# Performance work log

Measured on AMD Instinct MI355X. Metric: run time of the kernel, lower is better.

## Reference

```python
import jax, jax.numpy as jnp
import numpy as np

B, H, W = 2, 256, 256
C_BB = 1029          # concatenated deeplab backbone channels
FEATURE_DIM = 20     # output_conv emits FEATURE_DIM-5; +3 color +2 coords
NSPIX_H = NSPIX_W = 16
NSPIX = NSPIX_H * NSPIX_W
N_ITER = 10
HW = H * W


def _conv_bn_relu(x, Wc, g, b, eps=1e-5):
    # Conv2d(3x3, pad=1, bias=False) + BatchNorm2d (training stats) + ReLU
    y = jax.lax.conv_general_dilated(x, Wc, (1, 1), 'SAME',
                                     dimension_numbers=('NCHW', 'OIHW', 'NCHW'))
    mu = y.mean((0, 2, 3), keepdims=True)
    var = ((y - mu) ** 2).mean((0, 2, 3), keepdims=True)
    y = (y - mu) * jax.lax.rsqrt(var + eps)
    y = y * g.reshape(1, -1, 1, 1) + b.reshape(1, -1, 1, 1)
    return jnp.maximum(y, 0.0)


def _candidates():
    # init label map (nearest-neighbor upsample of the 16x16 superpixel grid)
    r0 = (jnp.arange(H) * NSPIX_H) // H
    c0 = (jnp.arange(W) * NSPIX_W) // W
    d = jnp.array([-1, 0, 1])
    dr, dc = jnp.meshgrid(d, d, indexing='ij')   # 3x3 superpixel neighborhood
    dr = dr.reshape(9); dc = dc.reshape(9)
    cr = r0[None, :, None] + dr[:, None, None]   # [9,H,1]
    cc = c0[None, None, :] + dc[:, None, None]   # [9,1,W]
    valid = (cr >= 0) & (cr < NSPIX_H) & (cc >= 0) & (cc < NSPIX_W)
    cid = jnp.clip(cr, 0, NSPIX_H - 1) * NSPIX_W + jnp.clip(cc, 0, NSPIX_W - 1)
    cid = jnp.broadcast_to(cid, (9, H, W)).reshape(9, HW)
    valid = jnp.broadcast_to(valid, (9, H, W)).reshape(9, HW)
    return cid, valid


def _ssn_iter(pixel_f):
    Bq, C = pixel_f.shape[0], pixel_f.shape[1]
    cid, valid = _candidates()
    ids = cid.reshape(-1)                         # [9*HW]
    validf = valid[None].astype(pixel_f.dtype)    # [1,9,HW]
    pf = pixel_f.reshape(Bq, C, HW)
    pfT = pf.transpose(0, 2, 1)                   # [B,HW,C]
    # init centroids = adaptive_avg_pool2d to the superpixel grid
    cent = pixel_f.reshape(Bq, C, NSPIX_H, H // NSPIX_H, NSPIX_W, W // NSPIX_W).mean((3, 5)).reshape(Bq, C, NSPIX)
    neg_inf = jnp.asarray(-jnp.inf, pixel_f.dtype)

    def update(wb, pb):  # wb [9,HW], pb [HW,C] -> new centroids [C,K]
        dat = (wb[:, :, None] * pb[None, :, :]).reshape(9 * HW, C)
        num = jax.ops.segment_sum(dat, ids, num_segments=NSPIX)
        den = jax.ops.segment_sum(wb.reshape(-1), ids, num_segments=NSPIX)
        return (num / (den[:, None] + 1e-16)).T

    aff = None
    for _ in range(N_ITER):
        cc = cent[:, :, cid]                                      # [B,C,9,HW]
        dist = jnp.sum((pf[:, :, None, :] - cc) ** 2, axis=1)     # [B,9,HW]
        aff = jax.nn.softmax(jnp.where(valid[None], -dist, neg_inf), axis=1)
        w = aff * validf
        cent = jax.vmap(update)(w, pfT)
    return aff, cid, cent


def setup_inputs() -> dict:
    key = jax.random.key(0)
    ks = jax.random.split(key, 6)
    x = jax.random.normal(ks[0], (B, 3, H, W), jnp.float32)
    yy, xx = jnp.meshgrid(jnp.arange(H, dtype=jnp.float32),
                          jnp.arange(W, dtype=jnp.float32), indexing='ij')
    coords = jnp.broadcast_to(jnp.stack([yy, xx])[None], (B, 2, H, W))
    feats = jax.random.normal(ks[1], (B, C_BB, H, W), jnp.float32)

    def cw(k, o, i):
        return jax.random.normal(k, (o, i, 3, 3), jnp.float32) * (1.0 / np.sqrt(9.0 * i))

    return dict(x=x, coords=coords, feats=feats,
                W1=cw(ks[2], 500, C_BB), g1=jnp.ones(500), b1=jnp.zeros(500),
                W2=cw(ks[3], 100, 500), g2=jnp.ones(100), b2=jnp.zeros(100),
                W3=cw(ks[4], FEATURE_DIM - 5, 100), g3=jnp.ones(FEATURE_DIM - 5), b3=jnp.zeros(FEATURE_DIM - 5))


def reference(x, coords, feats, W1, g1, b1, W2, g2, b2, W3, g3, b3):
    h = _conv_bn_relu(feats, W1, g1, b1)
    h = _conv_bn_relu(h, W2, g2, b2)
    h = _conv_bn_relu(h, W3, g3, b3)
    pixel_f = jnp.concatenate([h, x, coords], axis=1)  # [B,FEATURE_DIM,H,W]
    return _ssn_iter(pixel_f)
```

## Files before the change

### kernel.cpp

```cpp
#include <hip/hip_runtime.h>
#include <math.h>

#define kB 2
#define kH 256
#define kW 256
#define kHW 65536
#define kHp 258
#define kWp 258
#define kNSPIX 256
#define kC 20
#define kNITER 10

typedef unsigned int uint;
typedef unsigned short ushort;

using f32x4  = __attribute__((ext_vector_type(4))) float;
using bf16x8 = __attribute__((ext_vector_type(8))) __bf16;

__device__ __forceinline__ ushort f2bf(float f) {
    uint u = __float_as_uint(f);
    u = (u + 0x7FFFu + ((u >> 16) & 1u)) >> 16;
    return (ushort)u;
}
__device__ __forceinline__ float bf2f(uint h) {
    return __uint_as_float(h << 16);
}

__device__ __forceinline__ void gld16(const void* g, void* l) {
    __builtin_amdgcn_global_load_lds(
        (const __attribute__((address_space(1))) unsigned int*)g,
        (__attribute__((address_space(3))) unsigned int*)l, 16, 0, 0);
}

__global__ __launch_bounds__(256) void xtrans(
    const float* __restrict__ src, ushort* __restrict__ dst,
    int Cin_real, int Cin_pad)
{
    __shared__ float s[64][33];
    const int ci0 = blockIdx.x * 32;
    const int p0  = blockIdx.y * 64;
    const int b   = blockIdx.z;
    const int tid = threadIdx.x;
    for (int e = tid; e < 2048; e += 256) {
        int ci = e >> 6, px = e & 63;
        int cig = ci0 + ci;
        float v = 0.f;
        if (cig < Cin_real) v = src[((long)b * Cin_real + cig) * kHW + p0 + px];
        s[px][ci] = v;
    }
    __syncthreads();
    const int px = tid >> 2, g = tid & 3;
    uint4 o;
    o.x = (uint)f2bf(s[px][g*8+0]) | ((uint)f2bf(s[px][g*8+1]) << 16);
    o.y = (uint)f2bf(s[px][g*8+2]) | ((uint)f2bf(s[px][g*8+3]) << 16);
    o.z = (uint)f2bf(s[px][g*8+4]) | ((uint)f2bf(s[px][g*8+5]) << 16);
    o.w = (uint)f2bf(s[px][g*8+6]) | ((uint)f2bf(s[px][g*8+7]) << 16);
    const int y = p0 >> 8;
    const int x = (p0 & 255) + px;
    *(uint4*)(dst + ((long)(b * kHp + y + 1) * kWp + x + 1) * Cin_pad + ci0 + g * 8) = o;
}

__global__ __launch_bounds__(256) void wtrans(
    const float* __restrict__ W, ushort* __restrict__ Wt,
    int Cout_real, int Cin_real, int Cout_pad, int Cin_pad)
{
    long idx = (long)blockIdx.x * 256 + threadIdx.x;
    long total = (long)9 * Cout_pad * Cin_pad;
    if (idx >= total) return;
    int t   = (int)(idx / ((long)Cout_pad * Cin_pad));
    long r  = idx - (long)t * Cout_pad * Cin_pad;
    int co  = (int)(r / Cin_pad);
    int ci  = (int)(r - (long)co * Cin_pad);
    float v = 0.f;
    if (co < Cout_real && ci < Cin_real) v = W[((long)co * Cin_real + ci) * 9 + t];
    Wt[idx] = f2bf(v);
}

__global__ __launch_bounds__(256) void zero_border(ushort* __restrict__ buf, int Cpad)
{
    int e = blockIdx.x * 256 + threadIdx.x;
    if (e >= 1028) return;
    int gq = blockIdx.y;
    int b  = blockIdx.z;
    int y, x;
    if (e < 516) { y = (e < 258) ? 0 : 257; x = (e < 258) ? e : e - 258; }
    else         { int f = e - 516; y = 1 + (f >> 1); x = (f & 1) ? 257 : 0; }
    uint4 z = {0u, 0u, 0u, 0u};
    *(uint4*)(buf + ((long)(b * kHp + y) * kWp + x) * Cpad + (long)gq * 8) = z;
}

__global__ __launch_bounds__(256, 3) void conv_mfma(
    const ushort* __restrict__ Xt, const ushort* __restrict__ Wt,
    ushort* __restrict__ Yt, float* __restrict__ stats,
    int Cin_pad, int Cout_pad, int nkc)
{
    __shared__ __align__(16) ushort As[2][6144];
    __shared__ __align__(16) ushort Bs[2][4608];

    const int tid  = threadIdx.x;
    const int lane = tid & 63;
    const int wave = tid >> 6;
    const int l15  = lane & 15;
    const int quad = lane >> 4;
    const int co_w = (wave >> 1) * 32;
    const int px_w = (wave & 1) * 64;
    const int co0  = blockIdx.x * 64;
    const int py   = blockIdx.y >> 1;
    const int x0   = (blockIdx.y & 1) * 128;
    const int b    = blockIdx.z;
    const int ca8  = (quad ^ ((l15 >> 1) & 3)) * 8;

    f32x4 acc[2][4];
    #pragma unroll
    for (int i = 0; i < 2; ++i)
        #pragma unroll
        for (int j = 0; j < 4; ++j) acc[i][j] = (f32x4)0.0f;

    auto stage = [&](int s, int kyv, int ci0) {
        const ushort* xrow = Xt + ((long)(b * kHp + py + kyv) * kWp + x0) * Cin_pad + ci0;
        ushort* bd = &Bs[s][0];
        {
            int u = tid;        int px = u >> 2, gs = u & 3;
            gld16(xrow + (long)px * Cin_pad + ((gs ^ ((px >> 1) & 3)) * 8), bd + u * 8);
        }
        {
            int u = tid + 256;  int px = u >> 2, gs = u & 3;
            gld16(xrow + (long)px * Cin_pad + ((gs ^ ((px >> 1) & 3)) * 8), bd + u * 8);
        }
        if (tid < 64) {
            int u = tid + 512;  int px = u >> 2; px = px > 129 ? 129 : px;
            int gs = u & 3;
            gld16(xrow + (long)px * Cin_pad + ((gs ^ ((px >> 1) & 3)) * 8), bd + u * 8);
        }
        const ushort* wb = Wt + ((long)(kyv * 3) * Cout_pad + co0) * Cin_pad + ci0;
        ushort* ad = &As[s][0];
        #pragma unroll
        for (int r = 0; r < 3; ++r) {
            int u = tid + r * 256;
            int tl = u >> 8, co = (u >> 2) & 63, gs = u & 3;
            gld16(wb + ((long)tl * Cout_pad + co) * Cin_pad + ((gs ^ ((co >> 1) & 3)) * 8), ad + u * 8);
        }
    };

    int ky = 0, cc = 0;
    stage(0, 0, 0);
    const int NCH = 3 * nkc;
    for (int q = 0; q < NCH; ++q) {
        const int s = q & 1;
        int ky_n = ky, cc_n = cc + 1;
        if (cc_n == nkc) { cc_n = 0; ++ky_n; }
        if (q + 1 < NCH) {
            stage(s ^ 1, ky_n, cc_n * 32);
            asm volatile("s_waitcnt vmcnt(5)" ::: "memory");
        } else {
            asm volatile("s_waitcnt vmcnt(0)" ::: "memory");
        }
        __builtin_amdgcn_s_barrier();
        asm volatile("" ::: "memory");

        const ushort* Ab = &As[s][0];
        const ushort* Bb = &Bs[s][0];
        #pragma unroll
        for (int kx = 0; kx < 3; ++kx) {
            bf16x8 a0 = *(const bf16x8*)(Ab + (kx * 64 + co_w + l15) * 32 + ca8);
            bf16x8 a1 = *(const bf16x8*)(Ab + (kx * 64 + co_w + 16 + l15) * 32 + ca8);
            #pragma unroll
            for (int j = 0; j < 4; ++j) {
                int px = px_w + j * 16 + l15 + kx;
                bf16x8 bb = *(const bf16x8*)(Bb + px * 32 + ((quad ^ ((px >> 1) & 3)) * 8));
                acc[0][j] = __builtin_amdgcn_mfma_f32_16x16x32_bf16(a0, bb, acc[0][j], 0, 0, 0);
                acc[1][j] = __builtin_amdgcn_mfma_f32_16x16x32_bf16(a1, bb, acc[1][j], 0, 0, 0);
            }
        }
        asm volatile("s_waitcnt lgkmcnt(0)" ::: "memory");
        __builtin_amdgcn_s_barrier();
        asm volatile("" ::: "memory");
        ky = ky_n; cc = cc_n;
    }

    const long rowbase = (long)(b * kHp + py + 1) * kWp + x0 + 1 + px_w;
    #pragma unroll
    for (int i = 0; i < 2; ++i) {
        #pragma unroll
        for (int reg = 0; reg < 4; ++reg) {
            int co_r = co0 + co_w + i * 16 + quad * 4 + reg;
            float s = 0.f, s2 = 0.f;
            #pragma unroll
            for (int j = 0; j < 4; ++j) {
                float v = acc[i][j][reg];
                s += v;
                s2 = fmaf(v, v, s2);
                Yt[(rowbase + j * 16 + l15) * Cout_pad + co_r] = f2bf(v);
            }
            #pragma unroll
            for (int off = 1; off <= 8; off <<= 1) {
                s  += __shfl_xor(s, off);
                s2 += __shfl_xor(s2, off);
            }
            if (l15 == 0) {
                atomicAdd(&stats[co_r], s);
                atomicAdd(&stats[Cout_pad + co_r], s2);
            }
        }
    }
}

__global__ void finalize_stats(const float* __restrict__ stats,
                               float* __restrict__ murs, int Cout_pad)
{
    int c = blockIdx.x * 256 + threadIdx.x;
    if (c >= Cout_pad) return;
    const float invN = 1.0f / (float)(kB * kHW);
    float mu  = stats[c] * invN;
    float var = stats[Cout_pad + c] * invN - mu * mu;
    murs[c] = mu;
    murs[Cout_pad + c] = rsqrtf(var + 1e-5f);
}

__global__ __launch_bounds__(256) void bn_relu_nhwc(
    ushort* __restrict__ Y, const float* __restrict__ murs,
    const float* __restrict__ g, const float* __restrict__ bia,
    int C_real, int C_pad)
{
    long idx = (long)blockIdx.x * 256 + threadIdx.x;
    const int ngc = C_pad >> 3;
    long total = (long)kB * kHW * ngc;
    if (idx >= total) return;
    int cg = (int)(idx % ngc);
    long p  = idx / ngc;
    int b  = (int)(p >> 16);
    int pp = (int)(p & 65535);
    int y = pp >> 8, x = pp & 255;
    ushort* ptr = Y + ((long)(b * kHp + y + 1) * kWp + x + 1) * C_pad + (long)cg * 8;
    uint4 v = *(uint4*)ptr;
    uint w[4] = {v.x, v.y, v.z, v.w};
    uint o[4];
    #pragma unroll
    for (int q = 0; q < 4; ++q) {
        int c0 = cg * 8 + q * 2;
        int c1 = c0 + 1;
        float f0 = 0.f, f1 = 0.f;
        if (c0 < C_real)
            f0 = fmaxf((bf2f(w[q] & 0xFFFFu) - murs[c0]) * murs[C_pad + c0] * g[c0] + bia[c0], 0.f);
        if (c1 < C_real)
            f1 = fmaxf((bf2f(w[q] >> 16) - murs[c1]) * murs[C_pad + c1] * g[c1] + bia[c1], 0.f);
        o[q] = (uint)f2bf(f0) | ((uint)f2bf(f1) << 16);
    }
    uint4 ov = {o[0], o[1], o[2], o[3]};
    *(uint4*)ptr = ov;
}

__global__ __launch_bounds__(256) void bn_to_pf(
    const ushort* __restrict__ y3, const float* __restrict__ murs,
    const float* __restrict__ g, const float* __restrict__ bia,
    float* __restrict__ pf)
{
    long idx = (long)blockIdx.x * 256 + threadIdx.x;
    if (idx >= (long)kB * 15 * kHW) return;
    int b  = (int)(idx / (15 * kHW));
    long r = idx - (long)b * 15 * kHW;
    int ch = (int)(r / kHW);
    long p = r - (long)ch * kHW;
    int y = (int)(p >> 8), x = (int)(p & 255);
    float v = bf2f((uint)y3[((long)(b * kHp + y + 1) * kWp + x + 1) * 64 + ch]);
    v = fmaxf((v - murs[ch]) * murs[64 + ch] * g[ch] + bia[ch], 0.f);
    pf[((long)b * kC + ch) * kHW + p] = v;
}

__global__ __launch_bounds__(256) void fill_extra(
    const float* __restrict__ x, const float* __restrict__ coords, float* __restrict__ pf)
{
    long idx = (long)blockIdx.x * 256 + threadIdx.x;
    if (idx >= (long)kB * 5 * kHW) return;
    int b   = (int)(idx / (5 * kHW));
    long rem = idx - (long)b * 5 * kHW;
    int c   = (int)(rem / kHW);
    long p  = rem - (long)c * kHW;
    float v = (c < 3) ? x[((long)b * 3 + c) * kHW + p]
                      : coords[((long)b * 2 + (c - 3)) * kHW + p];
    pf[((long)b * kC + 15 + c) * kHW + p] = v;
}

__global__ __launch_bounds__(256) void cid_kernel(float* __restrict__ out_cid)
{
    int idx = blockIdx.x * 256 + threadIdx.x;
    if (idx >= 9 * kHW) return;
    int k = idx / kHW, p = idx - k * kHW;
    int r = p >> 8, c = p & 255;
    int rr = (r >> 4) + k / 3 - 1;
    int cc = (c >> 4) + k % 3 - 1;
    rr = rr < 0 ? 0 : (rr > 15 ? 15 : rr);
    cc = cc < 0 ? 0 : (cc > 15 ? 15 : cc);
    out_cid[idx] = (float)(rr * 16 + cc);
}

__global__ __launch_bounds__(256) void cent_init(
    const float* __restrict__ pf, float* __restrict__ cent)
{
    int idx = blockIdx.x * 256 + threadIdx.x;
    if (idx >= kB * kC * kNSPIX) return;
    int b   = idx / (kC * kNSPIX);
    int rem = idx - b * (kC * kNSPIX);
    int c   = rem / kNSPIX;
    int s   = rem - c * kNSPIX;
    int sr = s >> 4, sc = s & 15;
    const float* base = pf + ((long)b * kC + c) * kHW;
    float sum = 0.f;
    for (int ry = 0; ry < 16; ++ry)
        for (int rx = 0; rx < 16; ++rx)
            sum += base[(sr * 16 + ry) * kW + sc * 16 + rx];
    cent[idx] = sum * (1.0f / 256.0f);
}

__global__ __launch_bounds__(256) void ssn_softmax(
    const float* __restrict__ pf, const float* __restrict__ cent, float* __restrict__ aff)
{
    __shared__ float s_cent[kC][kNSPIX];
    const int b   = blockIdx.y;
    const int tid = threadIdx.x;
    const float* cb = cent + (long)b * kC * kNSPIX;
    for (int i = tid; i < kC * kNSPIX; i += 256)
        s_cent[i >> 8][i & 255] = cb[i];
    __syncthreads();

    const int p  = blockIdx.x * 256 + tid;
    const int r  = p >> 8, c = p & 255;
    const int r0 = r >> 4, c0 = c >> 4;

    float f[kC];
    const float* pb = pf + (long)b * kC * kHW + p;
    #pragma unroll
    for (int ch = 0; ch < kC; ++ch) f[ch] = pb[(long)ch * kHW];

    float dist[9];
    bool  val[9];
    float mx = -1e30f;
    #pragma unroll
    for (int k = 0; k < 9; ++k) {
        int rr = r0 + k / 3 - 1;
        int cc = c0 + k % 3 - 1;
        bool v = (rr >= 0 && rr < 16 && cc >= 0 && cc < 16);
        val[k] = v;
        int sid = v ? rr * 16 + cc : 0;
        float d = 0.f;
        #pragma unroll
        for (int ch = 0; ch < kC; ++ch) {
            float t = f[ch] - s_cent[ch][sid];
            d = fmaf(t, t, d);
        }
        dist[k] = d;
        if (v) mx = fmaxf(mx, -d);
    }
    float e[9], sum = 0.f;
    #pragma unroll
    for (int k = 0; k < 9; ++k) {
        e[k] = val[k] ? expf(-dist[k] - mx) : 0.f;
        sum += e[k];
    }
    float inv = 1.0f / sum;
    float* ab = aff + (long)b * 9 * kHW + p;
    #pragma unroll
    for (int k = 0; k < 9; ++k) ab[(long)k * kHW] = e[k] * inv;
}

__global__ __launch_bounds__(256) void ssn_update(
    const float* __restrict__ pf, const float* __restrict__ aff, float* __restrict__ cent)
{
    const int b  = blockIdx.y;
    const int s  = blockIdx.x;
    const int sr = s >> 4, sc = s & 15;
    const int tid = threadIdx.x;
    const int ty = tid >> 4, tx = tid & 15;

    float acc[kC + 1];
    #pragma unroll
    for (int i = 0; i <= kC; ++i) acc[i] = 0.f;

    #pragma unroll
    for (int k = 0; k < 9; ++k) {
        int dr = k / 3 - 1, dc = k % 3 - 1;
        int br = sr - dr, bc = sc - dc;
        if (br < 0 || br > 15 || bc < 0 || bc > 15) continue;
        int p = (br * 16 + ty) * kW + bc * 16 + tx;
        float w = aff[((long)b * 9 + k) * kHW + p];
        const float* pb = pf + (long)b * kC * kHW + p;
        acc[kC] += w;
        #pragma unroll
        for (int ch = 0; ch < kC; ++ch)
            acc[ch] = fmaf(w, pb[(long)ch * kHW], acc[ch]);
    }

    #pragma unroll
    for (int off = 32; off >= 1; off >>= 1)
        #pragma unroll
        for (int ch = 0; ch <= kC; ++ch)
            acc[ch] += __shfl_down(acc[ch], off);

    __shared__ float part[4][kC + 1];
    int wid = tid >> 6;
    if ((tid & 63) == 0)
        #pragma unroll
        for (int ch = 0; ch <= kC; ++ch) part[wid][ch] = acc[ch];
    __syncthreads();
    if (tid < kC) {
        float num = part[0][tid] + part[1][tid] + part[2][tid] + part[3][tid];
        float den = part[0][kC] + part[1][kC] + part[2][kC] + part[3][kC];
        cent[((long)b * kC + tid) * kNSPIX + s] = num / (den + 1e-16f);
    }
}

extern "C" void kernel_launch(void* const* d_in, const int* in_sizes, int n_in,
                              void* d_out, int out_size, void* d_ws, size_t ws_size,
                              hipStream_t stream)
{
    const float* x      = (const float*)d_in[0];
    const float* coords = (const float*)d_in[1];
    const float* feats  = (const float*)d_in[2];
    const float* W1 = (const float*)d_in[3];
    const float* g1 = (const float*)d_in[4];
    const float* b1 = (const float*)d_in[5];
    const float* W2 = (const float*)d_in[6];
    const float* g2 = (const float*)d_in[7];
    const float* b2 = (const float*)d_in[8];
    const float* W3 = (const float*)d_in[9];
    const float* g3 = (const float*)d_in[10];
    const float* b3 = (const float*)d_in[11];

    const long HPWP = (long)kHp * kWp;
    char* ws = (char*)d_ws;
    ushort* Xt1 = (ushort*)ws;  ws += (long)kB * HPWP * 1056 * 2;
    ushort* Wt1 = (ushort*)ws;  ws += (long)9 * 512 * 1056 * 2;
    ushort* y1t = (ushort*)ws;  ws += (long)kB * HPWP * 512 * 2;
    ushort* Wt2 = (ushort*)ws;  ws += (long)9 * 128 * 512 * 2;
    ushort* y2t = (ushort*)ws;  ws += (long)kB * HPWP * 128 * 2;
    ushort* Wt3 = (ushort*)ws;  ws += (long)9 * 64 * 128 * 2;
    ushort* y3t = (ushort*)ws;  ws += (long)kB * HPWP * 64 * 2;
    float*  pf  = (float*)ws;   ws += (long)2 * kC * kHW * 4;
    float* stats1 = (float*)ws; ws += 1024 * 4;
    float* stats2 = (float*)ws; ws += 256 * 4;
    float* stats3 = (float*)ws; ws += 128 * 4;
    float* murs1  = (float*)ws; ws += 1024 * 4;
    float* murs2  = (float*)ws; ws += 256 * 4;
    float* murs3  = (float*)ws; ws += 128 * 4;

    hipMemsetAsync(stats1, 0, (1024 + 256 + 128 + 1024 + 256 + 128) * 4, stream);

    float* aff_out  = (float*)d_out;
    float* cid_out  = aff_out + (long)kB * 9 * kHW;
    float* cent_out = cid_out + (long)9 * kHW;

    zero_border<<<dim3(5, 132, kB), 256, 0, stream>>>(Xt1, 1056);
    zero_border<<<dim3(5,  64, kB), 256, 0, stream>>>(y1t, 512);
    zero_border<<<dim3(5,  16, kB), 256, 0, stream>>>(y2t, 128);

    xtrans<<<dim3(33, 1024, kB), 256, 0, stream>>>(feats, Xt1, 1029, 1056);
    wtrans<<<(int)(((long)9 * 512 * 1056 + 255) / 256), 256, 0, stream>>>(W1, Wt1, 500, 1029, 512, 1056);
    wtrans<<<(int)(((long)9 * 128 * 512 + 255) / 256), 256, 0, stream>>>(W2, Wt2, 100, 500, 128, 512);
    wtrans<<<(int)(((long)9 * 64 * 128 + 255) / 256), 256, 0, stream>>>(W3, Wt3, 15, 100, 64, 128);

    conv_mfma<<<dim3(8, 512, kB), 256, 0, stream>>>(Xt1, Wt1, y1t, stats1, 1056, 512, 33);
    finalize_stats<<<2, 256, 0, stream>>>(stats1, murs1, 512);
    bn_relu_nhwc<<<(int)(((long)kB * kHW * 64 + 255) / 256), 256, 0, stream>>>(y1t, murs1, g1, b1, 500, 512);

    conv_mfma<<<dim3(2, 512, kB), 256, 0, stream>>>(y1t, Wt2, y2t, stats2, 512, 128, 16);
    finalize_stats<<<1, 256, 0, stream>>>(stats2, murs2, 128);
    bn_relu_nhwc<<<(int)(((long)kB * kHW * 16 + 255) / 256), 256, 0, stream>>>(y2t, murs2, g2, b2, 100, 128);

    conv_mfma<<<dim3(1, 512, kB), 256, 0, stream>>>(y2t, Wt3, y3t, stats3, 128, 64, 4);
    finalize_stats<<<1, 256, 0, stream>>>(stats3, murs3, 64);
    bn_to_pf<<<(int)(((long)kB * 15 * kHW + 255) / 256), 256, 0, stream>>>(y3t, murs3, g3, b3, pf);

    fill_extra<<<(int)(((long)kB * 5 * kHW + 255) / 256), 256, 0, stream>>>(x, coords, pf);
    cid_kernel<<<(9 * kHW + 255) / 256, 256, 0, stream>>>(cid_out);
    cent_init<<<(kB * kC * kNSPIX + 255) / 256, 256, 0, stream>>>(pf, cent_out);

    for (int it = 0; it < kNITER; ++it) {
        ssn_softmax<<<dim3(kHW / 256, kB), 256, 0, stream>>>(pf, cent_out, aff_out);
        ssn_update<<<dim3(kNSPIX, kB), 256, 0, stream>>>(pf, aff_out, cent_out);
    }
}
```

Before: 3.856 ms.

## Enlarge conv MFMA tiles to full-row 128-channel blocks, vectorize stores and bn_to_pf

The implicit-GEMM conv kernel is templated on output-channel block and wave count. Large layers now use 512-thread blocks covering a full 256-pixel row and 128 output channels, with each wave computing a 64x64 tile (4x4 MFMA accumulators). This raises arithmetic intensity per staged LDS tile and cuts redundant halo and weight loads, at the cost of more registers and LDS and lower occupancy. Output stores are packed into 8-byte writes, and bn_to_pf now reads all 15 channels of a pixel in vector loads instead of launching one thread per channel.

```diff
diff --git a/kernel.cpp b/kernel.cpp
--- a/kernel.cpp
+++ b/kernel.cpp
@@ -89,56 +89,62 @@
     *(uint4*)(buf + ((long)(b * kHp + y) * kWp + x) * Cpad + (long)gq * 8) = z;
 }
 
-__global__ __launch_bounds__(256, 3) void conv_mfma(
+template<int CO_BLK, int NW>
+__global__ __launch_bounds__(NW * 64) void conv_mfma(
     const ushort* __restrict__ Xt, const ushort* __restrict__ Wt,
     ushort* __restrict__ Yt, float* __restrict__ stats,
     int Cin_pad, int Cout_pad, int nkc)
 {
-    __shared__ __align__(16) ushort As[2][6144];
-    __shared__ __align__(16) ushort Bs[2][4608];
+    constexpr int NT = NW * 64;
+    static_assert(CO_BLK * 4 == NT, "stage indexing assumes CO_BLK*4 == threads");
+    constexpr int ASLOT = 12 * CO_BLK;
+    constexpr int BSLOT = 1088;
+    constexpr int BPASS = 1024 / NT;
+    constexpr int VMC = BPASS + 3;
+
+    __shared__ __align__(16) ushort As[2][ASLOT * 8];
+    __shared__ __align__(16) ushort Bs[2][BSLOT * 8];
 
     const int tid  = threadIdx.x;
     const int lane = tid & 63;
-    const int wave = tid >> 6;
+    const int wid  = tid >> 6;
     const int l15  = lane & 15;
     const int quad = lane >> 4;
-    const int co_w = (wave >> 1) * 32;
-    const int px_w = (wave & 1) * 64;
-    const int co0  = blockIdx.x * 64;
-    const int py   = blockIdx.y >> 1;
-    const int x0   = (blockIdx.y & 1) * 128;
+    const int co_w = (wid >> 2) * 64;
+    const int px_w = (wid & 3) * 64;
+    const int co0  = blockIdx.x * CO_BLK;
+    const int py   = blockIdx.y;
     const int b    = blockIdx.z;
     const int ca8  = (quad ^ ((l15 >> 1) & 3)) * 8;
 
-    f32x4 acc[2][4];
-    #pragma unroll
-    for (int i = 0; i < 2; ++i)
+    f32x4 acc[4][4];
+    #pragma unroll
+    for (int i = 0; i < 4; ++i)
         #pragma unroll
         for (int j = 0; j < 4; ++j) acc[i][j] = (f32x4)0.0f;
 
     auto stage = [&](int s, int kyv, int ci0) {
-        const ushort* xrow = Xt + ((long)(b * kHp + py + kyv) * kWp + x0) * Cin_pad + ci0;
+        const ushort* xrow = Xt + (long)(b * kHp + py + kyv) * kWp * Cin_pad + ci0;
         ushort* bd = &Bs[s][0];
-        {
-            int u = tid;        int px = u >> 2, gs = u & 3;
+        #pragma unroll
+        for (int p = 0; p < BPASS; ++p) {
+            int u = tid + p * NT;
+            int px = u >> 2, gs = u & 3;
             gld16(xrow + (long)px * Cin_pad + ((gs ^ ((px >> 1) & 3)) * 8), bd + u * 8);
         }
-        {
-            int u = tid + 256;  int px = u >> 2, gs = u & 3;
-            gld16(xrow + (long)px * Cin_pad + ((gs ^ ((px >> 1) & 3)) * 8), bd + u * 8);
-        }
         if (tid < 64) {
-            int u = tid + 512;  int px = u >> 2; px = px > 129 ? 129 : px;
+            int u = 1024 + tid;
+            int px = u >> 2; px = px > 257 ? 257 : px;
             int gs = u & 3;
             gld16(xrow + (long)px * Cin_pad + ((gs ^ ((px >> 1) & 3)) * 8), bd + u * 8);
         }
         const ushort* wb = Wt + ((long)(kyv * 3) * Cout_pad + co0) * Cin_pad + ci0;
         ushort* ad = &As[s][0];
+        const int co = tid >> 2, gs = tid & 3;
+        const long srcv = (long)co * Cin_pad + ((gs ^ ((co >> 1) & 3)) * 8);
         #pragma unroll
         for (int r = 0; r < 3; ++r) {
-            int u = tid + r * 256;
-            int tl = u >> 8, co = (u >> 2) & 63, gs = u & 3;
-            gld16(wb + ((long)tl * Cout_pad + co) * Cin_pad + ((gs ^ ((co >> 1) & 3)) * 8), ad + u * 8);
+            gld16(wb + (long)r * Cout_pad * Cin_pad + srcv, ad + (tid + r * NT) * 8);
         }
     };
 
@@ -151,7 +157,7 @@
         if (cc_n == nkc) { cc_n = 0; ++ky_n; }
         if (q + 1 < NCH) {
             stage(s ^ 1, ky_n, cc_n * 32);
-            asm volatile("s_waitcnt vmcnt(5)" ::: "memory");
+            asm volatile("s_waitcnt vmcnt(%0)" :: "n"(VMC) : "memory");
         } else {
             asm volatile("s_waitcnt vmcnt(0)" ::: "memory");
         }
@@ -162,14 +168,17 @@
         const ushort* Bb = &Bs[s][0];
         #pragma unroll
         for (int kx = 0; kx < 3; ++kx) {
-            bf16x8 a0 = *(const bf16x8*)(Ab + (kx * 64 + co_w + l15) * 32 + ca8);
-            bf16x8 a1 = *(const bf16x8*)(Ab + (kx * 64 + co_w + 16 + l15) * 32 + ca8);
+            bf16x8 a[4];
+            #pragma unroll
+            for (int i = 0; i < 4; ++i)
+                a[i] = *(const bf16x8*)(Ab + (kx * CO_BLK + co_w + i * 16 + l15) * 32 + ca8);
             #pragma unroll
             for (int j = 0; j < 4; ++j) {
                 int px = px_w + j * 16 + l15 + kx;
                 bf16x8 bb = *(const bf16x8*)(Bb + px * 32 + ((quad ^ ((px >> 1) & 3)) * 8));
-                acc[0][j] = __builtin_amdgcn_mfma_f32_16x16x32_bf16(a0, bb, acc[0][j], 0, 0, 0);
-                acc[1][j] = __builtin_amdgcn_mfma_f32_16x16x32_bf16(a1, bb, acc[1][j], 0, 0, 0);
+                #pragma unroll
+                for (int i = 0; i < 4; ++i)
+                    acc[i][j] = __builtin_amdgcn_mfma_f32_16x16x32_bf16(a[i], bb, acc[i][j], 0, 0, 0);
             }
         }
         asm volatile("s_waitcnt lgkmcnt(0)" ::: "memory");
@@ -178,27 +187,33 @@
         ky = ky_n; cc = cc_n;
     }
 
-    const long rowbase = (long)(b * kHp + py + 1) * kWp + x0 + 1 + px_w;
-    #pragma unroll
-    for (int i = 0; i < 2; ++i) {
+    const long rowbase = (long)(b * kHp + py + 1) * kWp + 1 + px_w;
+    #pragma unroll
+    for (int i = 0; i < 4; ++i) {
+        #pragma unroll
+        for (int j = 0; j < 4; ++j) {
+            uint2 pk;
+            pk.x = (uint)f2bf(acc[i][j][0]) | ((uint)f2bf(acc[i][j][1]) << 16);
+            pk.y = (uint)f2bf(acc[i][j][2]) | ((uint)f2bf(acc[i][j][3]) << 16);
+            *(uint2*)(Yt + (rowbase + j * 16 + l15) * Cout_pad + co0 + co_w + i * 16 + quad * 4) = pk;
+        }
         #pragma unroll
         for (int reg = 0; reg < 4; ++reg) {
             int co_r = co0 + co_w + i * 16 + quad * 4 + reg;
-            float s = 0.f, s2 = 0.f;
+            float sv = 0.f, s2 = 0.f;
             #pragma unroll
             for (int j = 0; j < 4; ++j) {
                 float v = acc[i][j][reg];
-                s += v;
+                sv += v;
                 s2 = fmaf(v, v, s2);
-                Yt[(rowbase + j * 16 + l15) * Cout_pad + co_r] = f2bf(v);
             }
             #pragma unroll
             for (int off = 1; off <= 8; off <<= 1) {
-                s  += __shfl_xor(s, off);
+                sv += __shfl_xor(sv, off);
                 s2 += __shfl_xor(s2, off);
             }
             if (l15 == 0) {
-                atomicAdd(&stats[co_r], s);
+                atomicAdd(&stats[co_r], sv);
                 atomicAdd(&stats[Cout_pad + co_r], s2);
             }
         }
@@ -256,15 +271,21 @@
     float* __restrict__ pf)
 {
     long idx = (long)blockIdx.x * 256 + threadIdx.x;
-    if (idx >= (long)kB * 15 * kHW) return;
-    int b  = (int)(idx / (15 * kHW));
-    long r = idx - (long)b * 15 * kHW;
-    int ch = (int)(r / kHW);
-    long p = r - (long)ch * kHW;
-    int y = (int)(p >> 8), x = (int)(p & 255);
-    float v = bf2f((uint)y3[((long)(b * kHp + y + 1) * kWp + x + 1) * 64 + ch]);
-    v = fmaxf((v - murs[ch]) * murs[64 + ch] * g[ch] + bia[ch], 0.f);
-    pf[((long)b * kC + ch) * kHW + p] = v;
+    if (idx >= (long)kB * kHW) return;
+    int b = (int)(idx >> 16);
+    int p = (int)(idx & 65535);
+    int y = p >> 8, x = p & 255;
+    const ushort* src = y3 + ((long)(b * kHp + y + 1) * kWp + x + 1) * 64;
+    uint4 v0 = *(const uint4*)src;
+    uint4 v1 = *(const uint4*)(src + 8);
+    uint wv[8] = {v0.x, v0.y, v0.z, v0.w, v1.x, v1.y, v1.z, v1.w};
+    #pragma unroll
+    for (int ch = 0; ch < 15; ++ch) {
+        uint h = (ch & 1) ? (wv[ch >> 1] >> 16) : (wv[ch >> 1] & 0xFFFFu);
+        float v = bf2f(h);
+        v = fmaxf((v - murs[ch]) * murs[64 + ch] * g[ch] + bia[ch], 0.f);
+        pf[((long)b * kC + ch) * kHW + p] = v;
+    }
 }
 
 __global__ __launch_bounds__(256) void fill_extra(
@@ -458,17 +479,17 @@
     wtrans<<<(int)(((long)9 * 128 * 512 + 255) / 256), 256, 0, stream>>>(W2, Wt2, 100, 500, 128, 512);
     wtrans<<<(int)(((long)9 * 64 * 128 + 255) / 256), 256, 0, stream>>>(W3, Wt3, 15, 100, 64, 128);
 
-    conv_mfma<<<dim3(8, 512, kB), 256, 0, stream>>>(Xt1, Wt1, y1t, stats1, 1056, 512, 33);
+    conv_mfma<128, 8><<<dim3(4, 256, kB), 512, 0, stream>>>(Xt1, Wt1, y1t, stats1, 1056, 512, 33);
     finalize_stats<<<2, 256, 0, stream>>>(stats1, murs1, 512);
     bn_relu_nhwc<<<(int)(((long)kB * kHW * 64 + 255) / 256), 256, 0, stream>>>(y1t, murs1, g1, b1, 500, 512);
 
-    conv_mfma<<<dim3(2, 512, kB), 256, 0, stream>>>(y1t, Wt2, y2t, stats2, 512, 128, 16);
+    conv_mfma<128, 8><<<dim3(1, 256, kB), 512, 0, stream>>>(y1t, Wt2, y2t, stats2, 512, 128, 16);
     finalize_stats<<<1, 256, 0, stream>>>(stats2, murs2, 128);
     bn_relu_nhwc<<<(int)(((long)kB * kHW * 16 + 255) / 256), 256, 0, stream>>>(y2t, murs2, g2, b2, 100, 128);
 
-    conv_mfma<<<dim3(1, 512, kB), 256, 0, stream>>>(y2t, Wt3, y3t, stats3, 128, 64, 4);
+    conv_mfma<64, 4><<<dim3(1, 256, kB), 256, 0, stream>>>(y2t, Wt3, y3t, stats3, 128, 64, 4);
     finalize_stats<<<1, 256, 0, stream>>>(stats3, murs3, 64);
-    bn_to_pf<<<(int)(((long)kB * 15 * kHW + 255) / 256), 256, 0, stream>>>(y3t, murs3, g3, b3, pf);
+    bn_to_pf<<<(int)(((long)kB * kHW + 255) / 256), 256, 0, stream>>>(y3t, murs3, g3, b3, pf);
 
     fill_extra<<<(int)(((long)kB * 5 * kHW + 255) / 256), 256, 0, stream>>>(x, coords, pf);
     cid_kernel<<<(9 * kHW + 255) / 256, 256, 0, stream>>>(cid_out);
```

Measured after the change: 4.014 ms. 4.1% more time.
